# Kernel optimization log

Measured on AMD Instinct MI355X. Metric: run time of the kernel, lower is better.

Reference implementation:

```python
import jax, jax.numpy as jnp
import numpy as np

H = 512  # hidden/input size
T = 16384
CLAMP_MAX = 49688.0

def setup_inputs() -> dict:
    key = jax.random.key(0)
    ks = jax.random.split(key, 12)
    s = 0.05
    x = jax.random.normal(ks[0], (T, 1, H), dtype=jnp.float32)
    W_ih = jax.random.normal(ks[1], (4 * H, H), dtype=jnp.float32) * s
    W_hh = jax.random.normal(ks[2], (4 * H, H), dtype=jnp.float32) * s
    b_ih = jax.random.normal(ks[3], (4 * H,), dtype=jnp.float32) * s
    b_hh = jax.random.normal(ks[4], (4 * H,), dtype=jnp.float32) * s
    fc_w = jax.random.normal(ks[5], (128, H), dtype=jnp.float32) * s
    fc_b = jax.random.normal(ks[6], (128,), dtype=jnp.float32) * s
    fc1_w = jax.random.normal(ks[7], (16, 128), dtype=jnp.float32) * s
    fc1_b = jax.random.normal(ks[8], (16,), dtype=jnp.float32) * s
    fc2_w = jax.random.normal(ks[9], (37, 128), dtype=jnp.float32) * s
    fc2_b = jax.random.normal(ks[10], (37,), dtype=jnp.float32) * s
    return {"x": x, "W_ih": W_ih, "W_hh": W_hh, "b_ih": b_ih, "b_hh": b_hh,
            "fc_w": fc_w, "fc_b": fc_b, "fc1_w": fc1_w, "fc1_b": fc1_b,
            "fc2_w": fc2_w, "fc2_b": fc2_b}

def _lstm(x, W_ih, W_hh, b_ih, b_hh):
    # x: [T, 1, H] seq-major, batch=1. Precompute input contribution for all t.
    xf = x.reshape(-1, H)                       # [T, H]
    x_gates = xf @ W_ih.T + (b_ih + b_hh)       # [T, 4H]

    def step(carry, xg):
        h, c = carry                            # [H], [H]
        g = xg + W_hh @ h                       # [4H]
        i = jax.nn.sigmoid(g[:H])
        f = jax.nn.sigmoid(g[H:2 * H])
        gg = jnp.tanh(g[2 * H:3 * H])
        o = jax.nn.sigmoid(g[3 * H:])
        c = f * c + i * gg
        h = o * jnp.tanh(c)
        return (h, c), h

    h0 = jnp.zeros((H,), dtype=x.dtype)
    c0 = jnp.zeros((H,), dtype=x.dtype)
    _, hs = jax.lax.scan(step, (h0, c0), x_gates)  # hs: [T, H]
    return hs

def reference(x, W_ih, W_hh, b_ih, b_hh, fc_w, fc_b, fc1_w, fc1_b, fc2_w, fc2_b):
    hs = _lstm(x, W_ih, W_hh, b_ih, b_hh)       # [T, H]
    inter = hs @ fc_w.T + fc_b                  # [T, 128]
    action = jnp.clip(inter @ fc1_w.T + fc1_b, 0.0, CLAMP_MAX)  # [T, 16]
    obj = jnp.clip(inter @ fc2_w.T + fc2_b, 0.0, CLAMP_MAX)     # [T, 37]
    return (action, obj)
```

## Files before the change

### kernel.cpp

```cpp
#include <hip/hip_runtime.h>
#include <hip/hip_bf16.h>
#include <stdint.h>

#define T_LEN 16384
#define HDIM 512
#define G4 2048
#define CLAMP_MAXV 49688.0f

#define XG_OFF    0ull
#define HS_OFF    134217728ull
#define INTER_OFF 167772160ull
#define HREC_OFF  176160768ull
#define BSUM_OFF  176168960ull
#define WS_NEED   176177152ull

__global__ __launch_bounds__(256) void init_k(uint64_t* __restrict__ hrec,
                                              const float* __restrict__ b_ih,
                                              const float* __restrict__ b_hh,
                                              float* __restrict__ bsum) {
    int i = blockIdx.x * 256 + threadIdx.x;
    if (i < 1024) hrec[i] = 0ull;
    bsum[i] = b_ih[i] + b_hh[i];
}

__global__ __launch_bounds__(256) void gemm_abt(const float* __restrict__ A,
                                                const float* __restrict__ B,
                                                const float* __restrict__ bias,
                                                float* __restrict__ C,
                                                int N, int K) {
    __shared__ float As[16][68];
    __shared__ float Bs[16][68];
    const int tid = threadIdx.x;
    const int bm = blockIdx.x << 6, bn = blockIdx.y << 6;
    const int tx = tid & 15, ty = tid >> 4;
    const int lr = tid >> 2, lk = (tid & 3) << 2;
    float acc[4][4] = {};
    const float* Ap = A + (size_t)(bm + lr) * K + lk;
    const float* Bp = B + (size_t)(bn + lr) * K + lk;
    for (int kt = 0; kt < K; kt += 16) {
        float4 av = *(const float4*)(Ap + kt);
        float4 bv = *(const float4*)(Bp + kt);
        __syncthreads();
        As[lk + 0][lr] = av.x; As[lk + 1][lr] = av.y;
        As[lk + 2][lr] = av.z; As[lk + 3][lr] = av.w;
        Bs[lk + 0][lr] = bv.x; Bs[lk + 1][lr] = bv.y;
        Bs[lk + 2][lr] = bv.z; Bs[lk + 3][lr] = bv.w;
        __syncthreads();
#pragma unroll
        for (int kk = 0; kk < 16; ++kk) {
            float4 a4 = *(const float4*)&As[kk][ty << 2];
            float4 b4 = *(const float4*)&Bs[kk][tx << 2];
            acc[0][0] += a4.x * b4.x; acc[0][1] += a4.x * b4.y;
            acc[0][2] += a4.x * b4.z; acc[0][3] += a4.x * b4.w;
            acc[1][0] += a4.y * b4.x; acc[1][1] += a4.y * b4.y;
            acc[1][2] += a4.y * b4.z; acc[1][3] += a4.y * b4.w;
            acc[2][0] += a4.z * b4.x; acc[2][1] += a4.z * b4.y;
            acc[2][2] += a4.z * b4.z; acc[2][3] += a4.z * b4.w;
            acc[3][0] += a4.w * b4.x; acc[3][1] += a4.w * b4.y;
            acc[3][2] += a4.w * b4.z; acc[3][3] += a4.w * b4.w;
        }
    }
    const int col = bn + (tx << 2);
    float4 bv4 = *(const float4*)&bias[col];
#pragma unroll
    for (int i = 0; i < 4; ++i) {
        int row = bm + (ty << 2) + i;
        float4 o;
        o.x = acc[i][0] + bv4.x; o.y = acc[i][1] + bv4.y;
        o.z = acc[i][2] + bv4.z; o.w = acc[i][3] + bv4.w;
        *(float4*)&C[(size_t)row * N + col] = o;
    }
}

__global__ __launch_bounds__(512, 2) void lstm_scan(const float* __restrict__ W_hh,
                                                    const float* __restrict__ xg,
                                                    float* __restrict__ hs,
                                                    uint64_t* __restrict__ hrec) {
    __shared__ float h_lds[512];
    __shared__ float part[512];
    const int tid = threadIdx.x;
    const int wv = tid >> 6;
    const int lane = tid & 63;
    const int j = blockIdx.x;
    const int rowg = ((lane >> 4) << 9) | (j << 4) | (lane & 15);

    float4 w4[16];
    {
        const float4* wp = (const float4*)(W_hh + (size_t)rowg * HDIM + (wv << 6));
#pragma unroll
        for (int q = 0; q < 16; ++q) w4[q] = wp[q];
    }

    float c_reg = 0.f;
    for (int t = 0; t < T_LEN; ++t) {
        float xgv = 0.f;
        if (wv == 0) xgv = xg[(size_t)t * G4 + rowg];

        uint64_t* src = hrec + ((t & 1) << 9) + tid;
        uint64_t u;
        int guard = 0;
        do {
            u = __hip_atomic_load(src, __ATOMIC_RELAXED, __HIP_MEMORY_SCOPE_AGENT);
        } while ((uint32_t)(u >> 32) != (uint32_t)t && ++guard < (1 << 18));
        h_lds[tid] = __uint_as_float((uint32_t)u);
        __syncthreads();

        float ac0 = 0.f, ac1 = 0.f, ac2 = 0.f, ac3 = 0.f;
        const float* hp = h_lds + (wv << 6);
#pragma unroll
        for (int q = 0; q < 16; q += 4) {
            float4 h0 = *(const float4*)(hp + (q << 2));
            float4 h1 = *(const float4*)(hp + ((q + 1) << 2));
            float4 h2 = *(const float4*)(hp + ((q + 2) << 2));
            float4 h3 = *(const float4*)(hp + ((q + 3) << 2));
            ac0 += w4[q].x * h0.x + w4[q].y * h0.y + w4[q].z * h0.z + w4[q].w * h0.w;
            ac1 += w4[q + 1].x * h1.x + w4[q + 1].y * h1.y + w4[q + 1].z * h1.z + w4[q + 1].w * h1.w;
            ac2 += w4[q + 2].x * h2.x + w4[q + 2].y * h2.y + w4[q + 2].z * h2.z + w4[q + 2].w * h2.w;
            ac3 += w4[q + 3].x * h3.x + w4[q + 3].y * h3.y + w4[q + 3].z * h3.z + w4[q + 3].w * h3.w;
        }
        part[tid] = (ac0 + ac1) + (ac2 + ac3);
        __syncthreads();

        if (wv == 0) {
            float g = xgv;
#pragma unroll
            for (int ww = 0; ww < 8; ++ww) g += part[(ww << 6) | lane];
            bool isg = (lane >= 32) && (lane < 48);
            float y = isg ? (g + g) : g;
            float s = 1.f / (1.f + __expf(-y));
            float a = isg ? (s + s - 1.f) : s;
            float fa = __shfl_down(a, 16);
            float ga = __shfl_down(a, 32);
            float oa = __shfl_down(a, 48);
            if (lane < 16) {
                c_reg = fa * c_reg + a * ga;
                float e2 = __expf(-2.f * c_reg);
                float hv = oa * (2.f / (1.f + e2) - 1.f);
                hs[(size_t)t * HDIM + (j << 4) + lane] = hv;
                uint64_t pu = ((uint64_t)(uint32_t)(t + 1) << 32) |
                              (uint64_t)__float_as_uint(hv);
                __hip_atomic_store(hrec + (((t + 1) & 1) << 9) + (j << 4) + lane, pu,
                                   __ATOMIC_RELAXED, __HIP_MEMORY_SCOPE_AGENT);
            }
        }
    }
}

__global__ __launch_bounds__(256) void heads_k(const float* __restrict__ inter,
                                               const float* __restrict__ fc1w,
                                               const float* __restrict__ fc1b,
                                               const float* __restrict__ fc2w,
                                               const float* __restrict__ fc2b,
                                               float* __restrict__ out) {
    __shared__ float it[64][128];
    __shared__ float wt[128][56];
    __shared__ float bl[56];
    const int tid = threadIdx.x;
    const int t0 = blockIdx.x << 6;
    for (int q = tid; q < 64 * 32; q += 256) {
        int r = q >> 5, c4 = q & 31;
        *(float4*)&it[r][c4 << 2] =
            *(const float4*)&inter[(size_t)(t0 + r) * 128 + (c4 << 2)];
    }
    for (int q = tid; q < 53 * 32; q += 256) {
        int r = q >> 5, c4 = q & 31;
        float4 v = (r < 16) ? ((const float4*)&fc1w[r * 128])[c4]
                            : ((const float4*)&fc2w[(r - 16) * 128])[c4];
        int k = c4 << 2;
        wt[k + 0][r] = v.x; wt[k + 1][r] = v.y; wt[k + 2][r] = v.z; wt[k + 3][r] = v.w;
    }
    if (tid < 53) bl[tid] = (tid < 16) ? fc1b[tid] : fc2b[tid - 16];
    __syncthreads();
    const int c = tid & 63, rg = tid >> 6;
    if (c < 53) {
        float b = bl[c];
        for (int rr = 0; rr < 16; ++rr) {
            int r = (rg << 4) + rr;
            float acc = b;
#pragma unroll 8
            for (int k = 0; k < 128; k += 4) {
                float4 iv = *(const float4*)&it[r][k];
                acc += iv.x * wt[k][c] + iv.y * wt[k + 1][c] +
                       iv.z * wt[k + 2][c] + iv.w * wt[k + 3][c];
            }
            acc = fminf(fmaxf(acc, 0.f), CLAMP_MAXV);
            int t = t0 + r;
            if (c < 16) out[(size_t)t * 16 + c] = acc;
            else        out[262144 + (size_t)t * 37 + (c - 16)] = acc;
        }
    }
}

extern "C" void kernel_launch(void* const* d_in, const int* in_sizes, int n_in,
                              void* d_out, int out_size, void* d_ws, size_t ws_size,
                              hipStream_t stream) {
    const float* x     = (const float*)d_in[0];
    const float* W_ih  = (const float*)d_in[1];
    const float* W_hh  = (const float*)d_in[2];
    const float* b_ih  = (const float*)d_in[3];
    const float* b_hh  = (const float*)d_in[4];
    const float* fc_w  = (const float*)d_in[5];
    const float* fc_b  = (const float*)d_in[6];
    const float* fc1_w = (const float*)d_in[7];
    const float* fc1_b = (const float*)d_in[8];
    const float* fc2_w = (const float*)d_in[9];
    const float* fc2_b = (const float*)d_in[10];

    if (ws_size < WS_NEED) return;

    char* ws = (char*)d_ws;
    float*    xg    = (float*)(ws + XG_OFF);
    float*    hs    = (float*)(ws + HS_OFF);
    float*    inter = (float*)(ws + INTER_OFF);
    uint64_t* hrec  = (uint64_t*)(ws + HREC_OFF);
    float*    bsum  = (float*)(ws + BSUM_OFF);
    float*    out   = (float*)d_out;

    hipLaunchKernelGGL(init_k, dim3(8), dim3(256), 0, stream, hrec, b_ih, b_hh, bsum);
    hipLaunchKernelGGL(gemm_abt, dim3(256, 32), dim3(256), 0, stream,
                       x, W_ih, bsum, xg, 2048, 512);
    hipLaunchKernelGGL(lstm_scan, dim3(32), dim3(512), 0, stream, W_hh, xg, hs, hrec);
    hipLaunchKernelGGL(gemm_abt, dim3(256, 2), dim3(256), 0, stream,
                       hs, fc_w, fc_b, inter, 128, 512);
    hipLaunchKernelGGL(heads_k, dim3(256), dim3(256), 0, stream,
                       inter, fc1_w, fc1_b, fc2_w, fc2_b, out);
}
```

Measured before the change: 26.83 ms.

## Remap LSTM scan threads so gate reduction uses wave shuffles, dropping a barrier

Each wave now owns two hidden units. Lanes are split into 8-lane groups per gate, each covering a 64-wide K slice with a rotated float4 order. Partial dot products are reduced with xor shuffles instead of a shared-memory partial buffer, which removes the second __syncthreads per timestep and the serial 8-way sum in wave 0. The h buffer is double-buffered so the next step's LDS write cannot race with this step's reads. Every wave now loads xg and computes activations, which adds redundant transcendental work and global loads per step.

```diff
diff --git a/kernel.cpp b/kernel.cpp
--- a/kernel.cpp
+++ b/kernel.cpp
@@ -76,25 +76,29 @@
                                                     const float* __restrict__ xg,
                                                     float* __restrict__ hs,
                                                     uint64_t* __restrict__ hrec) {
-    __shared__ float h_lds[512];
-    __shared__ float part[512];
+    __shared__ __align__(16) float h_lds[2][512];
     const int tid = threadIdx.x;
     const int wv = tid >> 6;
     const int lane = tid & 63;
     const int j = blockIdx.x;
-    const int rowg = ((lane >> 4) << 9) | (j << 4) | (lane & 15);
+    const int hi = lane >> 5;
+    const int gate = (lane >> 3) & 3;
+    const int s = lane & 7;
+    const int hidx = (j << 4) | (wv << 1) | hi;
+    const int rowg = (gate << 9) | hidx;
 
     float4 w4[16];
     {
-        const float4* wp = (const float4*)(W_hh + (size_t)rowg * HDIM + (wv << 6));
-#pragma unroll
-        for (int q = 0; q < 16; ++q) w4[q] = wp[q];
-    }
-
+        const float4* wp = (const float4*)(W_hh + (size_t)rowg * HDIM + (s << 6));
+#pragma unroll
+        for (int q = 0; q < 16; ++q) w4[q] = wp[(q + s) & 15];
+    }
+
+    const int fbase = s << 4;
+    const bool isg = (gate == 2);
     float c_reg = 0.f;
     for (int t = 0; t < T_LEN; ++t) {
-        float xgv = 0.f;
-        if (wv == 0) xgv = xg[(size_t)t * G4 + rowg];
+        float xgv = xg[(size_t)t * G4 + rowg];
 
         uint64_t* src = hrec + ((t & 1) << 9) + tid;
         uint64_t u;
@@ -102,46 +106,47 @@
         do {
             u = __hip_atomic_load(src, __ATOMIC_RELAXED, __HIP_MEMORY_SCOPE_AGENT);
         } while ((uint32_t)(u >> 32) != (uint32_t)t && ++guard < (1 << 18));
-        h_lds[tid] = __uint_as_float((uint32_t)u);
+        float* hb = h_lds[t & 1];
+        hb[tid] = __uint_as_float((uint32_t)u);
         __syncthreads();
 
+        const float4* h4p = (const float4*)hb;
         float ac0 = 0.f, ac1 = 0.f, ac2 = 0.f, ac3 = 0.f;
-        const float* hp = h_lds + (wv << 6);
 #pragma unroll
         for (int q = 0; q < 16; q += 4) {
-            float4 h0 = *(const float4*)(hp + (q << 2));
-            float4 h1 = *(const float4*)(hp + ((q + 1) << 2));
-            float4 h2 = *(const float4*)(hp + ((q + 2) << 2));
-            float4 h3 = *(const float4*)(hp + ((q + 3) << 2));
+            float4 h0 = h4p[fbase | ((q + 0 + s) & 15)];
+            float4 h1 = h4p[fbase | ((q + 1 + s) & 15)];
+            float4 h2 = h4p[fbase | ((q + 2 + s) & 15)];
+            float4 h3 = h4p[fbase | ((q + 3 + s) & 15)];
             ac0 += w4[q].x * h0.x + w4[q].y * h0.y + w4[q].z * h0.z + w4[q].w * h0.w;
             ac1 += w4[q + 1].x * h1.x + w4[q + 1].y * h1.y + w4[q + 1].z * h1.z + w4[q + 1].w * h1.w;
             ac2 += w4[q + 2].x * h2.x + w4[q + 2].y * h2.y + w4[q + 2].z * h2.z + w4[q + 2].w * h2.w;
             ac3 += w4[q + 3].x * h3.x + w4[q + 3].y * h3.y + w4[q + 3].z * h3.z + w4[q + 3].w * h3.w;
         }
-        part[tid] = (ac0 + ac1) + (ac2 + ac3);
-        __syncthreads();
-
-        if (wv == 0) {
-            float g = xgv;
-#pragma unroll
-            for (int ww = 0; ww < 8; ++ww) g += part[(ww << 6) | lane];
-            bool isg = (lane >= 32) && (lane < 48);
-            float y = isg ? (g + g) : g;
-            float s = 1.f / (1.f + __expf(-y));
-            float a = isg ? (s + s - 1.f) : s;
-            float fa = __shfl_down(a, 16);
-            float ga = __shfl_down(a, 32);
-            float oa = __shfl_down(a, 48);
-            if (lane < 16) {
-                c_reg = fa * c_reg + a * ga;
-                float e2 = __expf(-2.f * c_reg);
-                float hv = oa * (2.f / (1.f + e2) - 1.f);
-                hs[(size_t)t * HDIM + (j << 4) + lane] = hv;
-                uint64_t pu = ((uint64_t)(uint32_t)(t + 1) << 32) |
-                              (uint64_t)__float_as_uint(hv);
-                __hip_atomic_store(hrec + (((t + 1) & 1) << 9) + (j << 4) + lane, pu,
-                                   __ATOMIC_RELAXED, __HIP_MEMORY_SCOPE_AGENT);
-            }
+        float v = (ac0 + ac1) + (ac2 + ac3);
+        v += __shfl_xor(v, 1);
+        v += __shfl_xor(v, 2);
+        v += __shfl_xor(v, 4);
+        float g = v + xgv;
+
+        float y = isg ? (g + g) : g;
+        float sg = 1.f / (1.f + __expf(-y));
+        float a = isg ? (sg + sg - 1.f) : sg;
+
+        float fa = __shfl_down(a, 8);
+        float ga = __shfl_down(a, 16);
+        float oa = __shfl_down(a, 24);
+
+        c_reg = fa * c_reg + a * ga;
+        float e2 = __expf(-2.f * c_reg);
+        float hv = oa * (2.f / (1.f + e2) - 1.f);
+
+        if ((lane & 31) == 0) {
+            uint64_t pu = ((uint64_t)(uint32_t)(t + 1) << 32) |
+                          (uint64_t)__float_as_uint(hv);
+            __hip_atomic_store(hrec + (((t + 1) & 1) << 9) + hidx, pu,
+                               __ATOMIC_RELAXED, __HIP_MEMORY_SCOPE_AGENT);
+            hs[(size_t)t * HDIM + hidx] = hv;
         }
     }
 }
```

Measured after the change: 37.65 ms. 40.3% more time.
